# Kernel tuning notes

Hardware: AMD Instinct MI355X
Metric: run time of the kernel (lower is better)

## Reference

```python
import math
import jax, jax.numpy as jnp
import numpy as np

N_EMBD = 1024
N_HEAD = 16
B, T = 2, 2048
MASK_VALUE = -1000000.0


def setup_inputs() -> dict:
    key = jax.random.key(0)
    ks = jax.random.split(key, 10)
    s = 1.0 / math.sqrt(N_EMBD)
    x = jax.random.normal(ks[0], (B, T, N_EMBD), dtype=jnp.float32)
    # torch.nn.Linear weights are (out_features, in_features)
    Wq = jax.random.normal(ks[1], (N_EMBD, N_EMBD), dtype=jnp.float32) * s
    bq = jax.random.normal(ks[2], (N_EMBD,), dtype=jnp.float32) * s
    Wk = jax.random.normal(ks[3], (N_EMBD, N_EMBD), dtype=jnp.float32) * s
    bk = jax.random.normal(ks[4], (N_EMBD,), dtype=jnp.float32) * s
    Wv = jax.random.normal(ks[5], (N_EMBD, N_EMBD), dtype=jnp.float32) * s
    bv = jax.random.normal(ks[6], (N_EMBD,), dtype=jnp.float32) * s
    Wp = jax.random.normal(ks[7], (N_EMBD, N_EMBD), dtype=jnp.float32) * s
    bp = jax.random.normal(ks[8], (N_EMBD,), dtype=jnp.float32) * s
    # causal attn mask (B, T, T): 1 where attention allowed
    attn_mask = jnp.broadcast_to(
        jnp.tril(jnp.ones((T, T), dtype=jnp.int32))[None], (B, T, T))
    valid_input_mask = jnp.ones((B, T), dtype=jnp.int32)
    return {"x": x, "Wq": Wq, "bq": bq, "Wk": Wk, "bk": bk,
            "Wv": Wv, "bv": bv, "Wp": Wp, "bp": bp,
            "attn_mask": attn_mask, "valid_input_mask": valid_input_mask}


def reference(x, Wq, bq, Wk, bk, Wv, bv, Wp, bp, attn_mask, valid_input_mask):
    Bb, Tt, C = x.shape
    H = N_HEAD
    d = C // H
    # projections (torch Linear: x @ W.T + b), split into heads -> (B, H, T, d)
    def heads(y):
        return y.reshape(Bb, Tt, H, d).transpose(0, 2, 1, 3)
    q = heads(x @ Wq.T + bq)
    k = heads(x @ Wk.T + bk)
    v = heads(x @ Wv.T + bv)
    # attention scores (B, H, T, T)
    att = jnp.einsum('bhtd,bhsd->bhts', q, k) * (1.0 / math.sqrt(d))
    att = jnp.where(attn_mask[:, None, :, :] == 0, MASK_VALUE, att)
    att = jnp.where(valid_input_mask[:, None, None, :] == 0, MASK_VALUE, att)
    att = jax.nn.softmax(att, axis=-1)
    y = jnp.einsum('bhts,bhsd->bhtd', att, v)
    y = y.transpose(0, 2, 1, 3).reshape(Bb, Tt, C)
    return y @ Wp.T + bp
```

## Files before the change

### kernel.cpp

```cpp
#include <hip/hip_runtime.h>
#include <hip/hip_bf16.h>
#include <stdint.h>

typedef unsigned short u16;
typedef __attribute__((ext_vector_type(8))) short bf16x8;
typedef __attribute__((ext_vector_type(4))) float f32x4;

#define AS1 __attribute__((address_space(1)))
#define AS3 __attribute__((address_space(3)))

__device__ __forceinline__ void gload_lds16(const void* g, void* l) {
  __builtin_amdgcn_global_load_lds((const AS1 void*)g, (AS3 void*)l, 16, 0, 0);
}

__device__ __forceinline__ u16 f2bf(float f) {
  union { float f; uint32_t u; } v; v.f = f;
  uint32_t r = v.u + 0x7FFFu + ((v.u >> 16) & 1u);
  return (u16)(r >> 16);
}

__global__ void cvt_all(const float* __restrict__ x,
                        const float* __restrict__ w0, const float* __restrict__ w1,
                        const float* __restrict__ w2, const float* __restrict__ w3,
                        u16* __restrict__ x16, u16* __restrict__ w16) {
  int i = blockIdx.x * 256 + threadIdx.x;
  const float* src; u16* dst; int off;
  if (i < 1048576) { src = x; dst = x16; off = i; }
  else {
    int j = i - 1048576; int w = j >> 18; off = j & 262143;
    src = (w == 0) ? w0 : (w == 1) ? w1 : (w == 2) ? w2 : w3;
    dst = w16 + (size_t)w * 1048576;
  }
  float4 v = ((const float4*)src)[off];
  uint64_t pk = (uint64_t)f2bf(v.x) | ((uint64_t)f2bf(v.y) << 16) |
                ((uint64_t)f2bf(v.z) << 32) | ((uint64_t)f2bf(v.w) << 48);
  ((uint64_t*)dst)[off] = pk;
}

#define BM 128
#define BN 128
#define BK 32

template<int MODE>
__global__ __launch_bounds__(256, 2)
void gemm_bt(const u16* __restrict__ A, const u16* __restrict__ Bw,
             const float* __restrict__ bias0, const float* __restrict__ bias1,
             const float* __restrict__ bias2, void* __restrict__ Out,
             int M, int N, int K)
{
  __shared__ __align__(16) u16 As[BM * BK];
  __shared__ __align__(16) u16 Bs[BN * BK];
  const int tid = threadIdx.x;
  const int lane = tid & 63, wid = tid >> 6;
  const int lr = lane & 15, lg = lane >> 4;
  const int id = blockIdx.x;
  const int cpx = gridDim.x >> 3;
  const int swz = (id & 7) * cpx + (id >> 3);
  const int z = swz >> 8;
  const int rem = swz & 255;
  const int m0 = (rem >> 3) * BM, n0 = (rem & 7) * BN;
  const u16* Bz = Bw + (size_t)z * N * K;
  const float* bias = (MODE == 0) ? (z == 0 ? bias0 : (z == 1 ? bias1 : bias2)) : bias0;
  const int wm = (wid >> 1) * 64, wn = (wid & 1) * 64;

  f32x4 acc[4][4] = {};

  for (int kt = 0; kt < K; kt += BK) {
    __syncthreads();
#pragma unroll
    for (int i = 0; i < 2; ++i) {
      int cb = (i * 4 + wid) * 64;
      int c = cb + lane;
      int row = c >> 2, kc = (c & 3) * 8;
      gload_lds16(A  + (size_t)(m0 + row) * K + kt + kc, (void*)&As[(size_t)cb * 8]);
      gload_lds16(Bz + (size_t)(n0 + row) * K + kt + kc, (void*)&Bs[(size_t)cb * 8]);
    }
    __syncthreads();

    bf16x8 af[4], bfr[4];
#pragma unroll
    for (int mf = 0; mf < 4; ++mf) af[mf]  = *(const bf16x8*)&As[(wm + mf * 16 + lr) * BK + lg * 8];
#pragma unroll
    for (int nf = 0; nf < 4; ++nf) bfr[nf] = *(const bf16x8*)&Bs[(wn + nf * 16 + lr) * BK + lg * 8];
#pragma unroll
    for (int mf = 0; mf < 4; ++mf)
#pragma unroll
      for (int nf = 0; nf < 4; ++nf)
        acc[mf][nf] = __builtin_amdgcn_mfma_f32_16x16x32_bf16(af[mf], bfr[nf], acc[mf][nf], 0, 0, 0);
  }

#pragma unroll
  for (int nf = 0; nf < 4; ++nf) {
    float bv = bias[n0 + wn + nf * 16 + lr];
#pragma unroll
    for (int mf = 0; mf < 4; ++mf)
#pragma unroll
      for (int r = 0; r < 4; ++r) {
        int m = m0 + wm + mf * 16 + lg * 4 + r;
        int n = n0 + wn + nf * 16 + lr;
        float v = acc[mf][nf][r] + bv;
        if (MODE == 0) {
          if (z == 0) v *= 0.125f;
          size_t addr = ((size_t)(m >> 11) * 16 + (n >> 6)) * (size_t)(2048 * 64)
                      + (size_t)(m & 2047) * 64 + (n & 63);
          ((u16*)Out)[(size_t)z * 4194304 + addr] = f2bf(v);
        } else {
          ((float*)Out)[(size_t)m * N + n] = v;
        }
      }
  }
}

__global__ void transpose_v(const u16* __restrict__ v, u16* __restrict__ vt) {
  __shared__ __align__(16) u16 t[64][72];
  const int tid = threadIdx.x;
  const int s0 = blockIdx.x * 64;
  const int bh = blockIdx.y;
  const u16* src = v + (size_t)bh * 2048 * 64;
  u16* dst = vt + (size_t)bh * 64 * 2048;
#pragma unroll
  for (int i = 0; i < 2; ++i) {
    int c = tid + i * 256;
    int r = c >> 3, col = (c & 7) * 8;
    *(bf16x8*)&t[r][col] = *(const bf16x8*)&src[(size_t)(s0 + r) * 64 + col];
  }
  __syncthreads();
#pragma unroll
  for (int i = 0; i < 2; ++i) {
    int c = tid + i * 256;
    int d = c >> 3, sc = (c & 7) * 8;
    bf16x8 o;
#pragma unroll
    for (int j = 0; j < 8; ++j) o[j] = (short)t[sc + j][d];
    *(bf16x8*)&dst[(size_t)d * 2048 + s0 + sc] = o;
  }
}

__global__ __launch_bounds__(512, 4)
void attn_fwd(const u16* __restrict__ q, const u16* __restrict__ k,
              const u16* __restrict__ vt, u16* __restrict__ y)
{
  __shared__ __align__(16) u16 Ks[128 * 64];
  __shared__ __align__(16) u16 Vs[64 * 128];
  __shared__ __align__(16) u16 Ps[8][16 * 136];
  const int tid = threadIdx.x, lane = tid & 63, wid = tid >> 6;
  const int lr = lane & 15, lg = lane >> 4;
  const int bx = blockIdx.x, by = blockIdx.y;
  const int r4 = (bx + by) & 15;
  const int qt = (by & 16) ? r4 : 15 - r4;
  const int q0 = qt * 128;
  const int bh = by;
  const u16* qg = q + (size_t)bh * 2048 * 64;
  const u16* kg = k + (size_t)bh * 2048 * 64;
  const u16* vg = vt + (size_t)bh * 64 * 2048;
  const int trow0 = q0 + wid * 16;
  const int tq = trow0 + lr;

  bf16x8 qa[2];
#pragma unroll
  for (int kk = 0; kk < 2; ++kk)
    qa[kk] = *(const bf16x8*)&qg[(size_t)(trow0 + lr) * 64 + kk * 32 + lg * 8];

  const int l8 = lane >> 3, s8 = lane & 7;
  const int kr0 = wid * 16 + l8;
  const int vd  = wid * 8 + l8;
  const u16* kld = kg + (size_t)kr0 * 64 + s8 * 8;
  const u16* vld = vg + (size_t)vd * 2048 + s8 * 8;
  u16* kst0 = &Ks[kr0 * 64 + (s8 ^ l8) * 8];
  u16* kst1 = &Ks[(kr0 + 8) * 64 + (s8 ^ l8) * 8];
  u16* vst0 = &Vs[vd * 128 + ((s8    ) ^ (vd & 7)) * 8];
  u16* vst1 = &Vs[vd * 128 + ((s8 + 8) ^ (vd & 7)) * 8];

  bf16x8 ldK0, ldK1, ldV0, ldV1;
  ldK0 = *(const bf16x8*)(kld);
  ldK1 = *(const bf16x8*)(kld + 8 * 64);
  ldV0 = *(const bf16x8*)(vld);
  ldV1 = *(const bf16x8*)(vld + 64);

  f32x4 oacc[4] = {};
  float mrun = -1e30f, lrun = 0.f;
  const int nk2 = qt + 1;
  const int xsl = lr & 7;

  for (int j = 0; j < nk2; ++j) {
    *(bf16x8*)kst0 = ldK0;  *(bf16x8*)kst1 = ldK1;
    *(bf16x8*)vst0 = ldV0;  *(bf16x8*)vst1 = ldV1;
    if (j + 1 < nk2) {
      const u16* kn = kld + (size_t)(j + 1) * 8192;
      const u16* vn = vld + (size_t)(j + 1) * 128;
      ldK0 = *(const bf16x8*)(kn);
      ldK1 = *(const bf16x8*)(kn + 8 * 64);
      ldV0 = *(const bf16x8*)(vn);
      ldV1 = *(const bf16x8*)(vn + 64);
    }
    asm volatile("s_waitcnt lgkmcnt(0)" ::: "memory");
    __builtin_amdgcn_s_barrier();

    f32x4 sacc[8] = {};
#pragma unroll
    for (int kk = 0; kk < 2; ++kk) {
#pragma unroll
      for (int h = 0; h < 2; ++h) {
        bf16x8 kb[4];
#pragma unroll
        for (int sf = 0; sf < 4; ++sf)
          kb[sf] = *(const bf16x8*)&Ks[((h * 4 + sf) * 16 + lr) * 64 + (((kk * 4 + lg) ^ xsl) * 8)];
#pragma unroll
        for (int sf = 0; sf < 4; ++sf)
          sacc[h * 4 + sf] = __builtin_amdgcn_mfma_f32_16x16x32_bf16(kb[sf], qa[kk], sacc[h * 4 + sf], 0, 0, 0);
      }
    }

    if (j == qt) {
#pragma unroll
      for (int sf = 0; sf < 8; ++sf)
#pragma unroll
        for (int r = 0; r < 4; ++r) {
          int s = j * 128 + sf * 16 + lg * 4 + r;
          if (s > tq) sacc[sf][r] = -1e30f;
        }
    }

    float m01 = fmaxf(fmaxf(fmaxf(sacc[0][0], sacc[0][1]), fmaxf(sacc[0][2], sacc[0][3])),
                      fmaxf(fmaxf(sacc[1][0], sacc[1][1]), fmaxf(sacc[1][2], sacc[1][3])));
    float m23 = fmaxf(fmaxf(fmaxf(sacc[2][0], sacc[2][1]), fmaxf(sacc[2][2], sacc[2][3])),
                      fmaxf(fmaxf(sacc[3][0], sacc[3][1]), fmaxf(sacc[3][2], sacc[3][3])));
    float m45 = fmaxf(fmaxf(fmaxf(sacc[4][0], sacc[4][1]), fmaxf(sacc[4][2], sacc[4][3])),
                      fmaxf(fmaxf(sacc[5][0], sacc[5][1]), fmaxf(sacc[5][2], sacc[5][3])));
    float m67 = fmaxf(fmaxf(fmaxf(sacc[6][0], sacc[6][1]), fmaxf(sacc[6][2], sacc[6][3])),
                      fmaxf(fmaxf(sacc[7][0], sacc[7][1]), fmaxf(sacc[7][2], sacc[7][3])));
    float mx = fmaxf(fmaxf(m01, m23), fmaxf(m45, m67));
    mx = fmaxf(mx, __shfl_xor(mx, 16));
    mx = fmaxf(mx, __shfl_xor(mx, 32));
    if (!__all(mx - mrun <= 8.0f)) {
      float mn = fmaxf(mrun, mx);
      float scn = __expf(mrun - mn);
      mrun = mn;
      lrun *= scn;
      float scr[4];
#pragma unroll
      for (int r = 0; r < 4; ++r) scr[r] = __shfl(scn, lg * 4 + r);
#pragma unroll
      for (int nf = 0; nf < 4; ++nf)
#pragma unroll
        for (int r = 0; r < 4; ++r) oacc[nf][r] *= scr[r];
    }
    float rs = 0.f;
#pragma unroll
    for (int sf = 0; sf < 8; ++sf)
#pragma unroll
      for (int r = 0; r < 4; ++r) {
        float p = __expf(sacc[sf][r] - mrun);
        sacc[sf][r] = p;
        rs += p;
      }
    rs += __shfl_xor(rs, 16);
    rs += __shfl_xor(rs, 32);
    lrun += rs;

#pragma unroll
    for (int sf = 0; sf < 8; ++sf) {
      union { ushort4 u; uint2 d; } pk_;
      pk_.u.x = f2bf(sacc[sf][0]); pk_.u.y = f2bf(sacc[sf][1]);
      pk_.u.z = f2bf(sacc[sf][2]); pk_.u.w = f2bf(sacc[sf][3]);
      *(uint2*)&Ps[wid][lr * 136 + sf * 16 + lg * 4] = pk_.d;
    }

#pragma unroll
    for (int kk = 0; kk < 4; ++kk) {
      bf16x8 pa = *(const bf16x8*)&Ps[wid][lr * 136 + kk * 32 + lg * 8];
      bf16x8 vb[4];
#pragma unroll
      for (int nf = 0; nf < 4; ++nf)
        vb[nf] = *(const bf16x8*)&Vs[(nf * 16 + lr) * 128 + (((kk * 4 + lg) ^ xsl) * 8)];
#pragma unroll
      for (int nf = 0; nf < 4; ++nf)
        oacc[nf] = __builtin_amdgcn_mfma_f32_16x16x32_bf16(pa, vb[nf], oacc[nf], 0, 0, 0);
    }

    asm volatile("s_waitcnt lgkmcnt(0)" ::: "memory");
    __builtin_amdgcn_s_barrier();
  }

  const int b = bh >> 4, h = bh & 15;
#pragma unroll
  for (int r = 0; r < 4; ++r) {
    float lshf = __shfl(lrun, lg * 4 + r);
    float inv = 1.f / lshf;
    int t = trow0 + lg * 4 + r;
#pragma unroll
    for (int nf = 0; nf < 4; ++nf) {
      int n = nf * 16 + lr;
      y[((size_t)b * 2048 + t) * 1024 + h * 64 + n] = f2bf(oacc[nf][r] * inv);
    }
  }
}

extern "C" void kernel_launch(void* const* d_in, const int* in_sizes, int n_in,
                              void* d_out, int out_size, void* d_ws, size_t ws_size,
                              hipStream_t stream) {
  const float* x  = (const float*)d_in[0];
  const float* Wq = (const float*)d_in[1];
  const float* bq = (const float*)d_in[2];
  const float* Wk = (const float*)d_in[3];
  const float* bk = (const float*)d_in[4];
  const float* Wv = (const float*)d_in[5];
  const float* bv = (const float*)d_in[6];
  const float* Wp = (const float*)d_in[7];
  const float* bp = (const float*)d_in[8];

  char* ws = (char*)d_ws;
  u16* x16  = (u16*)(ws + (size_t)0);
  u16* w16  = (u16*)(ws + ((size_t)8  << 20));
  u16* q16  = (u16*)(ws + ((size_t)16 << 20));
  u16* k16  = (u16*)(ws + ((size_t)24 << 20));
  u16* v16  = (u16*)(ws + ((size_t)32 << 20));
  u16* vt16 = (u16*)(ws + ((size_t)40 << 20));
  u16* y16  = x16;

  cvt_all<<<8192, 256, 0, stream>>>(x, Wq, Wk, Wv, Wp, x16, w16);
  gemm_bt<0><<<768, 256, 0, stream>>>(x16, w16, bq, bk, bv, (void*)q16, 4096, 1024, 1024);
  transpose_v<<<dim3(32, 32), 256, 0, stream>>>(v16, vt16);
  attn_fwd<<<dim3(16, 32), 512, 0, stream>>>(q16, k16, vt16, y16);
  gemm_bt<1><<<256, 256, 0, stream>>>(y16, w16 + 3 * 1048576, bp, bp, bp, d_out, 4096, 1024, 1024);
}
```

Before: 118.2 us.

## Stage K/V tiles via direct global-to-LDS loads with split K/V prefetch

After: 120.0 us. Within noise of the previous version (+1.5%).

```diff
diff --git a/kernel.cpp b/kernel.cpp
--- a/kernel.cpp
+++ b/kernel.cpp
@@ -136,7 +136,7 @@
   }
 }
 
-__global__ __launch_bounds__(512, 4)
+__global__ __launch_bounds__(512, 2)
 void attn_fwd(const u16* __restrict__ q, const u16* __restrict__ k,
               const u16* __restrict__ vt, u16* __restrict__ y)
 {
@@ -155,6 +155,7 @@
   const u16* vg = vt + (size_t)bh * 64 * 2048;
   const int trow0 = q0 + wid * 16;
   const int tq = trow0 + lr;
+  const int nkt = qt + 1;
 
   bf16x8 qa[2];
 #pragma unroll
@@ -162,38 +163,29 @@
     qa[kk] = *(const bf16x8*)&qg[(size_t)(trow0 + lr) * 64 + kk * 32 + lg * 8];
 
   const int l8 = lane >> 3, s8 = lane & 7;
-  const int kr0 = wid * 16 + l8;
-  const int vd  = wid * 8 + l8;
-  const u16* kld = kg + (size_t)kr0 * 64 + s8 * 8;
-  const u16* vld = vg + (size_t)vd * 2048 + s8 * 8;
-  u16* kst0 = &Ks[kr0 * 64 + (s8 ^ l8) * 8];
-  u16* kst1 = &Ks[(kr0 + 8) * 64 + (s8 ^ l8) * 8];
-  u16* vst0 = &Vs[vd * 128 + ((s8    ) ^ (vd & 7)) * 8];
-  u16* vst1 = &Vs[vd * 128 + ((s8 + 8) ^ (vd & 7)) * 8];
-
-  bf16x8 ldK0, ldK1, ldV0, ldV1;
-  ldK0 = *(const bf16x8*)(kld);
-  ldK1 = *(const bf16x8*)(kld + 8 * 64);
-  ldV0 = *(const bf16x8*)(vld);
-  ldV1 = *(const bf16x8*)(vld + 64);
+  const int lv = lane >> 4, cv = lane & 15;
+  const u16* ksrcA = kg + (size_t)(wid * 16 + l8) * 64 + (s8 ^ l8) * 8;
+  const u16* vsrcA = vg + (size_t)(wid * 8 + lv) * 2048 + (cv ^ lv) * 8;
+  const u16* vsrcB = vg + (size_t)(wid * 8 + 4 + lv) * 2048 + (cv ^ (4 + lv)) * 8;
+
+#define STAGE_K(t) do {                                                        \
+    gload_lds16(ksrcA + (size_t)(t) * 8192,       (void*)&Ks[wid * 1024]);     \
+    gload_lds16(ksrcA + (size_t)(t) * 8192 + 512, (void*)&Ks[wid * 1024 + 512]); \
+  } while (0)
+#define STAGE_V(t) do {                                                        \
+    gload_lds16(vsrcA + (size_t)(t) * 128, (void*)&Vs[wid * 1024]);            \
+    gload_lds16(vsrcB + (size_t)(t) * 128, (void*)&Vs[wid * 1024 + 512]);      \
+  } while (0)
 
   f32x4 oacc[4] = {};
   float mrun = -1e30f, lrun = 0.f;
-  const int nk2 = qt + 1;
   const int xsl = lr & 7;
 
-  for (int j = 0; j < nk2; ++j) {
-    *(bf16x8*)kst0 = ldK0;  *(bf16x8*)kst1 = ldK1;
-    *(bf16x8*)vst0 = ldV0;  *(bf16x8*)vst1 = ldV1;
-    if (j + 1 < nk2) {
-      const u16* kn = kld + (size_t)(j + 1) * 8192;
-      const u16* vn = vld + (size_t)(j + 1) * 128;
-      ldK0 = *(const bf16x8*)(kn);
-      ldK1 = *(const bf16x8*)(kn + 8 * 64);
-      ldV0 = *(const bf16x8*)(vn);
-      ldV1 = *(const bf16x8*)(vn + 64);
-    }
-    asm volatile("s_waitcnt lgkmcnt(0)" ::: "memory");
+  STAGE_K(0);
+  STAGE_V(0);
+
+  for (int j = 0; j < nkt; ++j) {
+    asm volatile("s_waitcnt vmcnt(0)" ::: "memory");
     __builtin_amdgcn_s_barrier();
 
     f32x4 sacc[8] = {};
@@ -210,6 +202,9 @@
           sacc[h * 4 + sf] = __builtin_amdgcn_mfma_f32_16x16x32_bf16(kb[sf], qa[kk], sacc[h * 4 + sf], 0, 0, 0);
       }
     }
+    asm volatile("s_waitcnt lgkmcnt(0)" ::: "memory");
+    __builtin_amdgcn_s_barrier();
+    if (j + 1 < nkt) STAGE_K(j + 1);
 
     if (j == qt) {
 #pragma unroll
@@ -280,7 +275,10 @@
 
     asm volatile("s_waitcnt lgkmcnt(0)" ::: "memory");
     __builtin_amdgcn_s_barrier();
-  }
+    if (j + 1 < nkt) STAGE_V(j + 1);
+  }
+#undef STAGE_K
+#undef STAGE_V
 
   const int b = bh >> 4, h = bh & 15;
 #pragma unroll
```

## Fuse V transpose into QKV GEMM epilogue and widen GEMM K-tile to 64

Applied to the files above, without the earlier changes.

Result: no change. 116.5 us (-1.5%).

```diff
diff --git a/kernel.cpp b/kernel.cpp
--- a/kernel.cpp
+++ b/kernel.cpp
@@ -39,17 +39,16 @@
 
 #define BM 128
 #define BN 128
-#define BK 32
 
 template<int MODE>
 __global__ __launch_bounds__(256, 2)
 void gemm_bt(const u16* __restrict__ A, const u16* __restrict__ Bw,
              const float* __restrict__ bias0, const float* __restrict__ bias1,
              const float* __restrict__ bias2, void* __restrict__ Out,
-             int M, int N, int K)
+             u16* __restrict__ VtOut, int M, int N, int K)
 {
-  __shared__ __align__(16) u16 As[BM * BK];
-  __shared__ __align__(16) u16 Bs[BN * BK];
+  __shared__ __align__(16) u16 As[BM * 64];
+  __shared__ __align__(16) u16 Bs[BN * 64];
   const int tid = threadIdx.x;
   const int lane = tid & 63, wid = tid >> 6;
   const int lr = lane & 15, lg = lane >> 4;
@@ -65,28 +64,57 @@
 
   f32x4 acc[4][4] = {};
 
-  for (int kt = 0; kt < K; kt += BK) {
+  for (int kt = 0; kt < K; kt += 64) {
     __syncthreads();
 #pragma unroll
-    for (int i = 0; i < 2; ++i) {
+    for (int i = 0; i < 4; ++i) {
       int cb = (i * 4 + wid) * 64;
       int c = cb + lane;
-      int row = c >> 2, kc = (c & 3) * 8;
+      int row = c >> 3, kc = (c & 7) * 8;
       gload_lds16(A  + (size_t)(m0 + row) * K + kt + kc, (void*)&As[(size_t)cb * 8]);
       gload_lds16(Bz + (size_t)(n0 + row) * K + kt + kc, (void*)&Bs[(size_t)cb * 8]);
     }
     __syncthreads();
 
-    bf16x8 af[4], bfr[4];
-#pragma unroll
-    for (int mf = 0; mf < 4; ++mf) af[mf]  = *(const bf16x8*)&As[(wm + mf * 16 + lr) * BK + lg * 8];
-#pragma unroll
-    for (int nf = 0; nf < 4; ++nf) bfr[nf] = *(const bf16x8*)&Bs[(wn + nf * 16 + lr) * BK + lg * 8];
-#pragma unroll
-    for (int mf = 0; mf < 4; ++mf)
-#pragma unroll
-      for (int nf = 0; nf < 4; ++nf)
-        acc[mf][nf] = __builtin_amdgcn_mfma_f32_16x16x32_bf16(af[mf], bfr[nf], acc[mf][nf], 0, 0, 0);
+#pragma unroll
+    for (int s = 0; s < 2; ++s) {
+      bf16x8 af[4], bfr[4];
+#pragma unroll
+      for (int mf = 0; mf < 4; ++mf) af[mf]  = *(const bf16x8*)&As[(wm + mf * 16 + lr) * 64 + s * 32 + lg * 8];
+#pragma unroll
+      for (int nf = 0; nf < 4; ++nf) bfr[nf] = *(const bf16x8*)&Bs[(wn + nf * 16 + lr) * 64 + s * 32 + lg * 8];
+#pragma unroll
+      for (int mf = 0; mf < 4; ++mf)
+#pragma unroll
+        for (int nf = 0; nf < 4; ++nf)
+          acc[mf][nf] = __builtin_amdgcn_mfma_f32_16x16x32_bf16(af[mf], bfr[nf], acc[mf][nf], 0, 0, 0);
+    }
+  }
+
+  if (MODE == 0 && z == 2) {
+    __syncthreads();
+    u16* tb = (wid < 2 ? As : Bs) + (wid & 1) * 4096;
+#pragma unroll
+    for (int nf = 0; nf < 4; ++nf) {
+      float bv = bias[n0 + wn + nf * 16 + lr];
+#pragma unroll
+      for (int mf = 0; mf < 4; ++mf)
+#pragma unroll
+        for (int r = 0; r < 4; ++r)
+          tb[(nf * 16 + lr) * 64 + (mf * 16 + lg * 4 + r)] = f2bf(acc[mf][nf][r] + bv);
+    }
+    asm volatile("s_waitcnt lgkmcnt(0)" ::: "memory");
+#pragma unroll
+    for (int c = 0; c < 8; ++c) {
+      int nl = c * 8 + (lane >> 3);
+      int mc = lane & 7;
+      bf16x8 vv = *(const bf16x8*)&tb[nl * 64 + mc * 8];
+      int ng = n0 + wn + nl;
+      int mg = m0 + wm + mc * 8;
+      size_t addr = (((size_t)(mg >> 11) * 16 + (ng >> 6)) * 64 + (ng & 63)) * 2048 + (mg & 2047);
+      *(bf16x8*)&VtOut[addr] = vv;
+    }
+    return;
   }
 
 #pragma unroll
@@ -108,31 +136,6 @@
           ((float*)Out)[(size_t)m * N + n] = v;
         }
       }
-  }
-}
-
-__global__ void transpose_v(const u16* __restrict__ v, u16* __restrict__ vt) {
-  __shared__ __align__(16) u16 t[64][72];
-  const int tid = threadIdx.x;
-  const int s0 = blockIdx.x * 64;
-  const int bh = blockIdx.y;
-  const u16* src = v + (size_t)bh * 2048 * 64;
-  u16* dst = vt + (size_t)bh * 64 * 2048;
-#pragma unroll
-  for (int i = 0; i < 2; ++i) {
-    int c = tid + i * 256;
-    int r = c >> 3, col = (c & 7) * 8;
-    *(bf16x8*)&t[r][col] = *(const bf16x8*)&src[(size_t)(s0 + r) * 64 + col];
-  }
-  __syncthreads();
-#pragma unroll
-  for (int i = 0; i < 2; ++i) {
-    int c = tid + i * 256;
-    int d = c >> 3, sc = (c & 7) * 8;
-    bf16x8 o;
-#pragma unroll
-    for (int j = 0; j < 8; ++j) o[j] = (short)t[sc + j][d];
-    *(bf16x8*)&dst[(size_t)d * 2048 + s0 + sc] = o;
   }
 }
 
@@ -314,13 +317,11 @@
   u16* w16  = (u16*)(ws + ((size_t)8  << 20));
   u16* q16  = (u16*)(ws + ((size_t)16 << 20));
   u16* k16  = (u16*)(ws + ((size_t)24 << 20));
-  u16* v16  = (u16*)(ws + ((size_t)32 << 20));
   u16* vt16 = (u16*)(ws + ((size_t)40 << 20));
   u16* y16  = x16;
 
   cvt_all<<<8192, 256, 0, stream>>>(x, Wq, Wk, Wv, Wp, x16, w16);
-  gemm_bt<0><<<768, 256, 0, stream>>>(x16, w16, bq, bk, bv, (void*)q16, 4096, 1024, 1024);
-  transpose_v<<<dim3(32, 32), 256, 0, stream>>>(v16, vt16);
+  gemm_bt<0><<<768, 256, 0, stream>>>(x16, w16, bq, bk, bv, (void*)q16, vt16, 4096, 1024, 1024);
   attn_fwd<<<dim3(16, 32), 512, 0, stream>>>(q16, k16, vt16, y16);
-  gemm_bt<1><<<256, 256, 0, stream>>>(y16, w16 + 3 * 1048576, bp, bp, bp, d_out, 4096, 1024, 1024);
-}
+  gemm_bt<1><<<256, 256, 0, stream>>>(y16, w16 + 3 * 1048576, bp, bp, bp, d_out, (u16*)nullptr, 4096, 1024, 1024);
+}
```
